# Kernel optimization log

Hardware: AMD Instinct MI355X
Metric: run time of the kernel (lower is better)

## Reference

```python
import jax, jax.numpy as jnp
import numpy as np

N, D, H, F = 50000, 128, 8, 512
HD = D // H
EPS_BN = 1e-5


def _batchnorm(x, gamma, beta):
    # BatchNorm1d in training mode: per-feature batch stats over node dim
    m = x.mean(axis=0)
    v = x.var(axis=0)
    return (x - m) * jax.lax.rsqrt(v + EPS_BN) * gamma + beta


def setup_inputs() -> dict:
    key = jax.random.key(0)
    ks = jax.random.split(key, 12)
    s = 0.05
    return {
        "src": jax.random.normal(ks[0], (N, D), jnp.float32),
        "edge_index": jax.random.randint(ks[1], (2, 800000), 0, N, jnp.int64),
        "q_w": jax.random.normal(ks[2], (D, D), jnp.float32) * s,
        "q_b": jnp.zeros((D,), jnp.float32),
        "k_w": jax.random.normal(ks[3], (D, D), jnp.float32) * s,
        "v_w": jax.random.normal(ks[4], (D, D), jnp.float32) * s,
        "out_w": jax.random.normal(ks[5], (D, D), jnp.float32) * s,
        "out_b": jnp.zeros((D,), jnp.float32),
        "g1": jnp.ones((D,), jnp.float32),
        "b1": jnp.zeros((D,), jnp.float32),
        "lin1_w": jax.random.normal(ks[6], (F, D), jnp.float32) * s,
        "lin1_b": jnp.zeros((F,), jnp.float32),
        "lin2_w": jax.random.normal(ks[7], (D, F), jnp.float32) * s,
        "lin2_b": jnp.zeros((D,), jnp.float32),
        "g2": jnp.ones((D,), jnp.float32),
        "b2": jnp.zeros((D,), jnp.float32),
    }


def reference(src, edge_index, q_w, q_b, k_w, v_w, out_w, out_b,
              g1, b1, lin1_w, lin1_b, lin2_w, lin2_b, g2, b2):
    n = src.shape[0]
    # add self loops, then attention edge index is (dst=edge[1], src=edge[0])
    loops = jnp.arange(n, dtype=edge_index.dtype)
    ei = jnp.concatenate([edge_index, jnp.stack([loops, loops])], axis=1)
    e_src, e_dst = ei[0], ei[1]  # message flows e_src -> e_dst; query index = e_dst

    scaling = float(HD) ** (-0.5)
    q = ((src @ q_w.T + q_b) * scaling).reshape(n, H, HD)
    k = (src @ k_w.T).reshape(n, H, HD)
    v = (src @ v_w.T).reshape(n, H, HD)

    # per-edge scores [E, H]
    w = jnp.einsum("ehd,ehd->eh", q[e_dst], k[e_src])
    # deterministic segment softmax over edges grouped by destination node
    mx = jax.ops.segment_max(w, e_dst, num_segments=n)
    ex = jnp.exp(w - mx[e_dst])
    den = jax.ops.segment_sum(ex, e_dst, num_segments=n)
    attn_w = ex / (den[e_dst] + 1e-16)  # [E, H]

    # weighted scatter-add aggregation -> [n, H, HD]
    msgs = attn_w[:, :, None] * v[e_src]
    agg = jax.ops.segment_sum(msgs, e_dst, num_segments=n)

    attn_out = agg.reshape(n, D) @ out_w.T + out_b
    x = _batchnorm(src + attn_out, g1, b1)

    ff = jax.nn.leaky_relu(x @ lin1_w.T + lin1_b, negative_slope=0.01)
    ff = ff @ lin2_w.T + lin2_b
    x = _batchnorm(x + ff, g2, b2)
    return x
```

## Files before the change

### kernel.cpp

```cpp
#include <hip/hip_runtime.h>
#include <math.h>

#define D 128
#define H 8
#define HD 16

typedef __attribute__((ext_vector_type(8))) short bf16x8;
typedef __attribute__((ext_vector_type(4))) float f32x4;

__device__ __forceinline__ ushort f2bf(float x) {
    union { float f; unsigned u; } v; v.f = x;
    unsigned r = v.u + 0x7fffu + ((v.u >> 16) & 1u);
    return (ushort)(r >> 16);
}
__device__ __forceinline__ float bflo(unsigned u) {
    union { unsigned u; float f; } x; x.u = u << 16; return x.f;
}
__device__ __forceinline__ float bfhi(unsigned u) {
    union { unsigned u; float f; } x; x.u = u & 0xffff0000u; return x.f;
}
__device__ __forceinline__ float bf2f(short s) {
    union { unsigned u; float f; } x; x.u = ((unsigned)(ushort)s) << 16; return x.f;
}

__device__ __forceinline__ float dot16(const float* qf, uint4 a, uint4 b) {
    float w;
    w  = qf[0]  * bflo(a.x) + qf[1]  * bfhi(a.x);
    w += qf[2]  * bflo(a.y) + qf[3]  * bfhi(a.y);
    w += qf[4]  * bflo(a.z) + qf[5]  * bfhi(a.z);
    w += qf[6]  * bflo(a.w) + qf[7]  * bfhi(a.w);
    w += qf[8]  * bflo(b.x) + qf[9]  * bfhi(b.x);
    w += qf[10] * bflo(b.y) + qf[11] * bfhi(b.y);
    w += qf[12] * bflo(b.z) + qf[13] * bfhi(b.z);
    w += qf[14] * bflo(b.w) + qf[15] * bfhi(b.w);
    return w;
}
__device__ __forceinline__ void acc16(float* num, float e, uint4 a, uint4 b) {
    num[0]  = fmaf(e, bflo(a.x), num[0]);  num[1]  = fmaf(e, bfhi(a.x), num[1]);
    num[2]  = fmaf(e, bflo(a.y), num[2]);  num[3]  = fmaf(e, bfhi(a.y), num[3]);
    num[4]  = fmaf(e, bflo(a.z), num[4]);  num[5]  = fmaf(e, bfhi(a.z), num[5]);
    num[6]  = fmaf(e, bflo(a.w), num[6]);  num[7]  = fmaf(e, bfhi(a.w), num[7]);
    num[8]  = fmaf(e, bflo(b.x), num[8]);  num[9]  = fmaf(e, bfhi(b.x), num[9]);
    num[10] = fmaf(e, bflo(b.y), num[10]); num[11] = fmaf(e, bfhi(b.y), num[11]);
    num[12] = fmaf(e, bflo(b.z), num[12]); num[13] = fmaf(e, bfhi(b.z), num[13]);
    num[14] = fmaf(e, bflo(b.w), num[14]); num[15] = fmaf(e, bfhi(b.w), num[15]);
}

template<int AMODE, int EPI, int K, int MW>
__global__ __launch_bounds__(256)
void gemm_v2_kernel(const void* __restrict__ Ap,
                    const ushort* __restrict__ W,
                    const float* __restrict__ bias,
                    const void* __restrict__ extra,
                    const float* __restrict__ stats,
                    ushort* __restrict__ outb,
                    int N)
{
    constexpr int M   = MW * 4;
    constexpr int KC  = (K < 128) ? K : 128;
    constexpr int KT  = KC / 32;
    constexpr int NKC = K / KC;

    const int lane = threadIdx.x & 63, wave = threadIdx.x >> 6;
    const int lr = lane & 15, lq = lane >> 4;
    const int row0 = blockIdx.x * 32;
    const int c0w  = wave * MW;

    int ar0 = row0 + lr;      if (ar0 > N - 1) ar0 = N - 1;
    int ar1 = row0 + 16 + lr; if (ar1 > N - 1) ar1 = N - 1;

    bf16x8 afr[2][KT];

    auto loadA = [&](int kc) {
        #pragma unroll
        for (int s = 0; s < 2; ++s) {
            int ar = s ? ar1 : ar0;
            if (AMODE == 0 || AMODE == 2) {
                const ushort* ap = (const ushort*)Ap + (size_t)ar * K + kc * KC + lq * 8;
                #pragma unroll
                for (int t = 0; t < KT; ++t) {
                    bf16x8 raw = *(const bf16x8*)(ap + t * 32);
                    if (AMODE == 0) {
                        afr[s][t] = raw;
                    } else {
                        int kb = kc * KC + t * 32 + lq * 8;
                        const float4* scp = (const float4*)(stats + 256 + kb);
                        const float4* shp = (const float4*)(stats + 384 + kb);
                        float4 sA = scp[0], sB = scp[1], hA = shp[0], hB = shp[1];
                        bf16x8 o;
                        o[0] = (short)f2bf(fmaf(bf2f(raw[0]), sA.x, hA.x));
                        o[1] = (short)f2bf(fmaf(bf2f(raw[1]), sA.y, hA.y));
                        o[2] = (short)f2bf(fmaf(bf2f(raw[2]), sA.z, hA.z));
                        o[3] = (short)f2bf(fmaf(bf2f(raw[3]), sA.w, hA.w));
                        o[4] = (short)f2bf(fmaf(bf2f(raw[4]), sB.x, hB.x));
                        o[5] = (short)f2bf(fmaf(bf2f(raw[5]), sB.y, hB.y));
                        o[6] = (short)f2bf(fmaf(bf2f(raw[6]), sB.z, hB.z));
                        o[7] = (short)f2bf(fmaf(bf2f(raw[7]), sB.w, hB.w));
                        afr[s][t] = o;
                    }
                }
            } else {
                const float* ap = (const float*)Ap + (size_t)ar * K + kc * KC + lq * 8;
                #pragma unroll
                for (int t = 0; t < KT; ++t) {
                    float4 f0 = *(const float4*)(ap + t * 32);
                    float4 f1 = *(const float4*)(ap + t * 32 + 4);
                    bf16x8 o;
                    o[0] = (short)f2bf(f0.x); o[1] = (short)f2bf(f0.y);
                    o[2] = (short)f2bf(f0.z); o[3] = (short)f2bf(f0.w);
                    o[4] = (short)f2bf(f1.x); o[5] = (short)f2bf(f1.y);
                    o[6] = (short)f2bf(f1.z); o[7] = (short)f2bf(f1.w);
                    afr[s][t] = o;
                }
            }
        }
    };

    if (NKC == 1) loadA(0);

    const float*  extf = (const float*)extra;
    const ushort* extb = (const ushort*)extra;

    #pragma unroll 1
    for (int cp = 0; cp < MW / 32; ++cp) {
        const int cbase = c0w + cp * 32;
        f32x4 acc[2][2] = {};

        #pragma unroll 1
        for (int kc = 0; kc < NKC; ++kc) {
            if (NKC > 1) loadA(kc);
            const ushort* wp0 = W + (size_t)(cbase + lr) * K + kc * KC + lq * 8;
            const ushort* wp1 = wp0 + (size_t)16 * K;
            #pragma unroll
            for (int t = 0; t < KT; ++t) {
                bf16x8 b0 = *(const bf16x8*)(wp0 + t * 32);
                bf16x8 b1 = *(const bf16x8*)(wp1 + t * 32);
                acc[0][0] = __builtin_amdgcn_mfma_f32_16x16x32_bf16(afr[0][t], b0, acc[0][0], 0, 0, 0);
                acc[1][0] = __builtin_amdgcn_mfma_f32_16x16x32_bf16(afr[1][t], b0, acc[1][0], 0, 0, 0);
                acc[0][1] = __builtin_amdgcn_mfma_f32_16x16x32_bf16(afr[0][t], b1, acc[0][1], 0, 0, 0);
                acc[1][1] = __builtin_amdgcn_mfma_f32_16x16x32_bf16(afr[1][t], b1, acc[1][1], 0, 0, 0);
            }
        }

        #pragma unroll
        for (int ct = 0; ct < 2; ++ct) {
            int col = cbase + ct * 16 + lr;
            float biasv = bias[col];
            float scv = 0.f, shv = 0.f;
            if (EPI == 4) { scv = stats[256 + col]; shv = stats[384 + col]; }
            #pragma unroll
            for (int s = 0; s < 2; ++s) {
                #pragma unroll
                for (int r = 0; r < 4; ++r) {
                    int grow = row0 + s * 16 + lq * 4 + r;
                    if (grow >= N) continue;
                    size_t o = (size_t)grow * M + col;
                    float v = acc[s][ct][r] + biasv;
                    if (EPI == 2) {
                        v = v > 0.f ? v : 0.01f * v;
                    } else if (EPI == 3) {
                        v += extf[o];
                    } else if (EPI == 4) {
                        v += fmaf(bf2f((short)extb[o]), scv, shv);
                    }
                    outb[o] = f2bf(v);
                }
            }
        }
    }
}

__global__ __launch_bounds__(256)
void convert_weights_kernel(const float* __restrict__ qw, const float* __restrict__ qb,
                            const float* __restrict__ kw, const float* __restrict__ vw,
                            const float* __restrict__ ow, const float* __restrict__ w1,
                            const float* __restrict__ w2,
                            ushort* __restrict__ wqkv, ushort* __restrict__ wout,
                            ushort* __restrict__ w1b, ushort* __restrict__ w2b,
                            float* __restrict__ bqkv)
{
    int i = blockIdx.x * 256 + threadIdx.x;
    if (i < 49152) {
        int row = i >> 7;
        float v;
        if (row < 128)      v = 0.25f * qw[i];
        else if (row < 256) v = kw[i - 16384];
        else                v = vw[i - 32768];
        wqkv[i] = f2bf(v);
        return;
    }
    int j = i - 49152;
    if (j < 16384) { wout[j] = f2bf(ow[j]); return; }
    j -= 16384;
    if (j < 65536) { w1b[j] = f2bf(w1[j]); return; }
    j -= 65536;
    if (j < 65536) { w2b[j] = f2bf(w2[j]); return; }
    j -= 65536;
    if (j < 384) bqkv[j] = (j < 128) ? 0.25f * qb[j] : 0.f;
}

__global__ __launch_bounds__(256)
void deg_count_kernel(const int* __restrict__ ei, long long E0, int* __restrict__ deg)
{
    long long e = (long long)blockIdx.x * 256 + threadIdx.x;
    if (e < E0) atomicAdd(&deg[ei[E0 + e]], 1);
}

__global__ __launch_bounds__(256)
void scan_block_sum(const int* __restrict__ deg, int n, int* __restrict__ bsum)
{
    __shared__ int sh[256];
    int i = blockIdx.x * 256 + threadIdx.x;
    sh[threadIdx.x] = (i < n) ? deg[i] : 0;
    __syncthreads();
    for (int ofs = 128; ofs > 0; ofs >>= 1) {
        if (threadIdx.x < ofs) sh[threadIdx.x] += sh[threadIdx.x + ofs];
        __syncthreads();
    }
    if (threadIdx.x == 0) bsum[blockIdx.x] = sh[0];
}

__global__ void scan_offsets(const int* __restrict__ bsum, int nb, int* __restrict__ boff)
{
    __shared__ int sh[256];
    int v = (threadIdx.x < nb) ? bsum[threadIdx.x] : 0;
    sh[threadIdx.x] = v;
    __syncthreads();
    for (int ofs = 1; ofs < 256; ofs <<= 1) {
        int t = (threadIdx.x >= ofs) ? sh[threadIdx.x - ofs] : 0;
        __syncthreads();
        sh[threadIdx.x] += t;
        __syncthreads();
    }
    if (threadIdx.x < nb) boff[threadIdx.x] = sh[threadIdx.x] - v;
}

__global__ __launch_bounds__(256)
void scan_final(const int* __restrict__ deg, int n, const int* __restrict__ boff,
                int* __restrict__ rowptr)
{
    __shared__ int sh[256];
    int i = blockIdx.x * 256 + threadIdx.x;
    int v = (i < n) ? deg[i] : 0;
    sh[threadIdx.x] = v;
    __syncthreads();
    for (int ofs = 1; ofs < 256; ofs <<= 1) {
        int t = (threadIdx.x >= ofs) ? sh[threadIdx.x - ofs] : 0;
        __syncthreads();
        sh[threadIdx.x] += t;
        __syncthreads();
    }
    if (i < n) rowptr[i] = boff[blockIdx.x] + sh[threadIdx.x] - v;
    if (i == n - 1) rowptr[n] = boff[blockIdx.x] + sh[threadIdx.x];
}

__global__ __launch_bounds__(256)
void scatter_kernel(const int* __restrict__ ei, long long E0,
                    const int* __restrict__ rowptr, int* __restrict__ cnt,
                    int* __restrict__ col)
{
    long long e = (long long)blockIdx.x * 256 + threadIdx.x;
    if (e >= E0) return;
    int s = ei[e], d = ei[E0 + e];
    int pos = rowptr[d] + atomicAdd(&cnt[d], 1);
    col[pos] = s;
}

__global__ __launch_bounds__(256)
void gat_agg_kernel(const int* __restrict__ rowptr, const int* __restrict__ col,
                    const ushort* __restrict__ qkv, ushort* __restrict__ agg, int NH)
{
    int t = blockIdx.x * 256 + threadIdx.x;
    if (t >= NH) return;
    int node = t >> 3, h = t & 7;
    const uint4* Q = (const uint4*)qkv;

    const uint4* qp = Q + (size_t)node * 48 + h * 2;
    uint4 qa = qp[0], qb = qp[1];
    float qf[16];
    qf[0]=bflo(qa.x); qf[1]=bfhi(qa.x); qf[2]=bflo(qa.y); qf[3]=bfhi(qa.y);
    qf[4]=bflo(qa.z); qf[5]=bfhi(qa.z); qf[6]=bflo(qa.w); qf[7]=bfhi(qa.w);
    qf[8]=bflo(qb.x); qf[9]=bfhi(qb.x); qf[10]=bflo(qb.y); qf[11]=bfhi(qb.y);
    qf[12]=bflo(qb.z); qf[13]=bfhi(qb.z); qf[14]=bflo(qb.w); qf[15]=bfhi(qb.w);

    float num[16];
    #pragma unroll
    for (int i = 0; i < 16; i++) num[i] = 0.f;
    float den = 0.f;

    {
        uint4 ka = qp[16], kb = qp[17], va = qp[32], vb = qp[33];
        float e = __expf(dot16(qf, ka, kb));
        den += e; acc16(num, e, va, vb);
    }

    int beg = rowptr[node], end = rowptr[node + 1];
    int j = beg;
    for (; j + 4 <= end; j += 4) {
        int s0 = col[j], s1 = col[j+1], s2 = col[j+2], s3 = col[j+3];
        const uint4* b0 = Q + (size_t)s0 * 48 + h * 2;
        const uint4* b1 = Q + (size_t)s1 * 48 + h * 2;
        const uint4* b2 = Q + (size_t)s2 * 48 + h * 2;
        const uint4* b3 = Q + (size_t)s3 * 48 + h * 2;
        uint4 ka0=b0[16], kb0=b0[17], va0=b0[32], vb0=b0[33];
        uint4 ka1=b1[16], kb1=b1[17], va1=b1[32], vb1=b1[33];
        uint4 ka2=b2[16], kb2=b2[17], va2=b2[32], vb2=b2[33];
        uint4 ka3=b3[16], kb3=b3[17], va3=b3[32], vb3=b3[33];
        float e0 = __expf(dot16(qf, ka0, kb0));
        float e1 = __expf(dot16(qf, ka1, kb1));
        float e2 = __expf(dot16(qf, ka2, kb2));
        float e3 = __expf(dot16(qf, ka3, kb3));
        den += e0 + e1 + e2 + e3;
        acc16(num, e0, va0, vb0); acc16(num, e1, va1, vb1);
        acc16(num, e2, va2, vb2); acc16(num, e3, va3, vb3);
    }
    for (; j < end; ++j) {
        int s = col[j];
        const uint4* bp = Q + (size_t)s * 48 + h * 2;
        uint4 ka = bp[16], kb = bp[17], va = bp[32], vb = bp[33];
        float e = __expf(dot16(qf, ka, kb));
        den += e; acc16(num, e, va, vb);
    }

    float inv = 1.f / (den + 1e-16f);
    uint4 o0, o1;
    o0.x = (uint)f2bf(num[0]*inv)  | ((uint)f2bf(num[1]*inv)  << 16);
    o0.y = (uint)f2bf(num[2]*inv)  | ((uint)f2bf(num[3]*inv)  << 16);
    o0.z = (uint)f2bf(num[4]*inv)  | ((uint)f2bf(num[5]*inv)  << 16);
    o0.w = (uint)f2bf(num[6]*inv)  | ((uint)f2bf(num[7]*inv)  << 16);
    o1.x = (uint)f2bf(num[8]*inv)  | ((uint)f2bf(num[9]*inv)  << 16);
    o1.y = (uint)f2bf(num[10]*inv) | ((uint)f2bf(num[11]*inv) << 16);
    o1.z = (uint)f2bf(num[12]*inv) | ((uint)f2bf(num[13]*inv) << 16);
    o1.w = (uint)f2bf(num[14]*inv) | ((uint)f2bf(num[15]*inv) << 16);
    uint4* op = reinterpret_cast<uint4*>(agg + (size_t)node * 128 + h * 16);
    op[0] = o0; op[1] = o1;
}

__global__ __launch_bounds__(256)
void bn_stats_bf16_kernel(const ushort* __restrict__ y, int N, float* __restrict__ stats)
{
    int jp = threadIdx.x & 63;
    int q4 = threadIdx.x >> 6;
    int r = blockIdx.x * 256 + q4;
    int rend = min(N, (int)(blockIdx.x + 1) * 256);
    float s0 = 0.f, qq0 = 0.f, s1 = 0.f, qq1 = 0.f;
    const uint* yp = (const uint*)y;
    for (; r < rend; r += 4) {
        uint u = yp[(size_t)r * 64 + jp];
        float a = bflo(u), b = bfhi(u);
        s0 += a; qq0 += a * a; s1 += b; qq1 += b * b;
    }
    __shared__ float sh[4][64][4];
    sh[q4][jp][0] = s0; sh[q4][jp][1] = qq0; sh[q4][jp][2] = s1; sh[q4][jp][3] = qq1;
    __syncthreads();
    if (threadIdx.x < 128) {
        int p = threadIdx.x >> 1;
        int w = threadIdx.x & 1;
        float ss = 0.f, sq = 0.f;
        #pragma unroll
        for (int i = 0; i < 4; i++) { ss += sh[i][p][w * 2]; sq += sh[i][p][w * 2 + 1]; }
        unsafeAtomicAdd(&stats[2 * p + w], ss);
        unsafeAtomicAdd(&stats[128 + 2 * p + w], sq);
    }
}

__global__ void bn_finalize_kernel(float* __restrict__ stats,
                                   const float* __restrict__ g,
                                   const float* __restrict__ b, int N)
{
    int j = threadIdx.x;
    float mean = stats[j] / (float)N;
    float var  = stats[128 + j] / (float)N - mean * mean;
    float sc = g[j] * rsqrtf(var + 1e-5f);
    stats[256 + j] = sc;
    stats[384 + j] = b[j] - mean * sc;
}

__global__ __launch_bounds__(256)
void bn_apply_out_kernel(const ushort* __restrict__ y, const float* __restrict__ stats,
                         float* __restrict__ out, int total4)
{
    int i = blockIdx.x * 256 + threadIdx.x;
    if (i >= total4) return;
    uint2 u = reinterpret_cast<const uint2*>(y)[i];
    int j = (i * 4) & (D - 1);
    float4 v;
    v.x = bflo(u.x) * stats[256 + j + 0] + stats[384 + j + 0];
    v.y = bfhi(u.x) * stats[256 + j + 1] + stats[384 + j + 1];
    v.z = bflo(u.y) * stats[256 + j + 2] + stats[384 + j + 2];
    v.w = bfhi(u.y) * stats[256 + j + 3] + stats[384 + j + 3];
    reinterpret_cast<float4*>(out)[i] = v;
}

extern "C" void kernel_launch(void* const* d_in, const int* in_sizes, int n_in,
                              void* d_out, int out_size, void* d_ws, size_t ws_size,
                              hipStream_t stream)
{
    const float* src    = (const float*)d_in[0];
    const int*   ei     = (const int*)  d_in[1];
    const float* q_w    = (const float*)d_in[2];
    const float* q_b    = (const float*)d_in[3];
    const float* k_w    = (const float*)d_in[4];
    const float* v_w    = (const float*)d_in[5];
    const float* out_w  = (const float*)d_in[6];
    const float* out_b  = (const float*)d_in[7];
    const float* g1     = (const float*)d_in[8];
    const float* b1     = (const float*)d_in[9];
    const float* lin1_w = (const float*)d_in[10];
    const float* lin1_b = (const float*)d_in[11];
    const float* lin2_w = (const float*)d_in[12];
    const float* lin2_b = (const float*)d_in[13];
    const float* g2     = (const float*)d_in[14];
    const float* b2     = (const float*)d_in[15];

    const int N        = in_sizes[0] / D;
    const long long E0 = in_sizes[1] / 2;

    float* ws = (float*)d_ws;
    size_t off = 0;
    ushort* qkv  = (ushort*)(ws + off); off += (size_t)N * 192;
    ushort* agg  = (ushort*)(ws + off); off += (size_t)N * 64;
    ushort* y1b  = (ushort*)(ws + off); off += (size_t)N * 64;
    ushort* hid  = (ushort*)(ws + off); off += (size_t)N * 256;
    ushort* y2b  = (ushort*)(ws + off); off += (size_t)N * 64;
    ushort* wqkv = (ushort*)(ws + off); off += 24576;
    ushort* woutb= (ushort*)(ws + off); off += 8192;
    ushort* w1b  = (ushort*)(ws + off); off += 32768;
    ushort* w2b  = (ushort*)(ws + off); off += 32768;
    float*  bqkv = ws + off;            off += 384;
    size_t zero_start = off;
    int* deg    = (int*)(ws + off); off += N;
    int* cnt    = (int*)(ws + off); off += N;
    float* stats1 = ws + off; off += 512;
    float* stats2 = ws + off; off += 512;
    size_t zero_cnt = off - zero_start;
    int* rowptr = (int*)(ws + off); off += N + 1;
    int* bsum   = (int*)(ws + off); off += 256;
    int* boff   = (int*)(ws + off); off += 256;
    int* col    = (int*)(ws + off); off += E0;

    hipMemsetAsync(ws + zero_start, 0, zero_cnt * sizeof(float), stream);

    dim3 blk(256);

    int cw_total = 49152 + 16384 + 65536 + 65536 + 384;
    hipLaunchKernelGGL(convert_weights_kernel, dim3((cw_total + 255) / 256), blk, 0, stream,
                       q_w, q_b, k_w, v_w, out_w, lin1_w, lin2_w,
                       wqkv, woutb, w1b, w2b, bqkv);

    dim3 gE0((unsigned)((E0 + 255) / 256));
    hipLaunchKernelGGL(deg_count_kernel, gE0, blk, 0, stream, ei, E0, deg);
    int nb = (N + 255) / 256;
    hipLaunchKernelGGL(scan_block_sum, dim3(nb), blk, 0, stream, deg, N, bsum);
    hipLaunchKernelGGL(scan_offsets, dim3(1), blk, 0, stream, bsum, nb, boff);
    hipLaunchKernelGGL(scan_final, dim3(nb), blk, 0, stream, deg, N, boff, rowptr);
    hipLaunchKernelGGL(scatter_kernel, gE0, blk, 0, stream, ei, E0, rowptr, cnt, col);

    dim3 gG((N + 31) / 32);

    hipLaunchKernelGGL((gemm_v2_kernel<1, 0, 128, 96>), gG, blk, 0, stream,
                       src, wqkv, bqkv, nullptr, nullptr, qkv, N);

    int NH = N * H;
    hipLaunchKernelGGL(gat_agg_kernel, dim3((NH + 255) / 256), blk, 0, stream,
                       rowptr, col, qkv, agg, NH);

    hipLaunchKernelGGL((gemm_v2_kernel<0, 3, 128, 32>), gG, blk, 0, stream,
                       agg, woutb, out_b, src, nullptr, y1b, N);

    dim3 gS((N + 255) / 256);
    hipLaunchKernelGGL(bn_stats_bf16_kernel, gS, blk, 0, stream, y1b, N, stats1);
    hipLaunchKernelGGL(bn_finalize_kernel, dim3(1), dim3(128), 0, stream, stats1, g1, b1, N);

    hipLaunchKernelGGL((gemm_v2_kernel<2, 2, 128, 128>), gG, blk, 0, stream,
                       y1b, w1b, lin1_b, nullptr, stats1, hid, N);
    hipLaunchKernelGGL((gemm_v2_kernel<0, 4, 512, 32>), gG, blk, 0, stream,
                       hid, w2b, lin2_b, y1b, stats1, y2b, N);

    hipLaunchKernelGGL(bn_stats_bf16_kernel, gS, blk, 0, stream, y2b, N, stats2);
    hipLaunchKernelGGL(bn_finalize_kernel, dim3(1), dim3(128), 0, stream, stats2, g2, b2, N);
    int total4 = N * D / 4;
    hipLaunchKernelGGL(bn_apply_out_kernel, dim3((total4 + 255) / 256), blk, 0, stream,
                       y2b, stats2, (float*)d_out, total4);
}
```

Baseline: 477.2 us.

## Split each node's edges across eight lane groups and fuse the scan kernels

```diff
diff --git a/kernel.cpp b/kernel.cpp
--- a/kernel.cpp
+++ b/kernel.cpp
@@ -66,8 +66,8 @@
     const int row0 = blockIdx.x * 32;
     const int c0w  = wave * MW;
 
-    int ar0 = row0 + lr;      if (ar0 > N - 1) ar0 = N - 1;
-    int ar1 = row0 + 16 + lr; if (ar1 > N - 1) ar1 = N - 1;
+    int ar0 = min(row0 + lr, N - 1);
+    int ar1 = min(row0 + 16 + lr, N - 1);
 
     bf16x8 afr[2][KT];
 
@@ -220,38 +220,35 @@
     if (threadIdx.x == 0) bsum[blockIdx.x] = sh[0];
 }
 
-__global__ void scan_offsets(const int* __restrict__ bsum, int nb, int* __restrict__ boff)
-{
+__global__ __launch_bounds__(256)
+void scan_final(const int* __restrict__ deg, int n, const int* __restrict__ bsum,
+                int nb, int* __restrict__ rowptr)
+{
+    __shared__ int sb[256];
     __shared__ int sh[256];
-    int v = (threadIdx.x < nb) ? bsum[threadIdx.x] : 0;
-    sh[threadIdx.x] = v;
+    int t = threadIdx.x;
+    sb[t] = (t < nb) ? bsum[t] : 0;
     __syncthreads();
     for (int ofs = 1; ofs < 256; ofs <<= 1) {
-        int t = (threadIdx.x >= ofs) ? sh[threadIdx.x - ofs] : 0;
+        int v = (t >= ofs) ? sb[t - ofs] : 0;
         __syncthreads();
-        sh[threadIdx.x] += t;
+        sb[t] += v;
         __syncthreads();
     }
-    if (threadIdx.x < nb) boff[threadIdx.x] = sh[threadIdx.x] - v;
-}
-
-__global__ __launch_bounds__(256)
-void scan_final(const int* __restrict__ deg, int n, const int* __restrict__ boff,
-                int* __restrict__ rowptr)
-{
-    __shared__ int sh[256];
-    int i = blockIdx.x * 256 + threadIdx.x;
+    int boff = (blockIdx.x == 0) ? 0 : sb[blockIdx.x - 1];
+
+    int i = blockIdx.x * 256 + t;
     int v = (i < n) ? deg[i] : 0;
-    sh[threadIdx.x] = v;
+    sh[t] = v;
     __syncthreads();
     for (int ofs = 1; ofs < 256; ofs <<= 1) {
-        int t = (threadIdx.x >= ofs) ? sh[threadIdx.x - ofs] : 0;
+        int u = (t >= ofs) ? sh[t - ofs] : 0;
         __syncthreads();
-        sh[threadIdx.x] += t;
+        sh[t] += u;
         __syncthreads();
     }
-    if (i < n) rowptr[i] = boff[blockIdx.x] + sh[threadIdx.x] - v;
-    if (i == n - 1) rowptr[n] = boff[blockIdx.x] + sh[threadIdx.x];
+    if (i < n) rowptr[i] = boff + sh[t] - v;
+    if (i == n - 1) rowptr[n] = boff + sh[t];
 }
 
 __global__ __launch_bounds__(256)
@@ -268,11 +265,12 @@
 
 __global__ __launch_bounds__(256)
 void gat_agg_kernel(const int* __restrict__ rowptr, const int* __restrict__ col,
-                    const ushort* __restrict__ qkv, ushort* __restrict__ agg, int NH)
-{
-    int t = blockIdx.x * 256 + threadIdx.x;
-    if (t >= NH) return;
-    int node = t >> 3, h = t & 7;
+                    const ushort* __restrict__ qkv, ushort* __restrict__ agg, int N)
+{
+    int node = blockIdx.x * 4 + (threadIdx.x >> 6);
+    if (node >= N) return;
+    int lane = threadIdx.x & 63;
+    int es = lane >> 3, h = lane & 7;
     const uint4* Q = (const uint4*)qkv;
 
     const uint4* qp = Q + (size_t)node * 48 + h * 2;
@@ -288,52 +286,38 @@
     for (int i = 0; i < 16; i++) num[i] = 0.f;
     float den = 0.f;
 
-    {
-        uint4 ka = qp[16], kb = qp[17], va = qp[32], vb = qp[33];
-        float e = __expf(dot16(qf, ka, kb));
-        den += e; acc16(num, e, va, vb);
-    }
-
-    int beg = rowptr[node], end = rowptr[node + 1];
-    int j = beg;
-    for (; j + 4 <= end; j += 4) {
-        int s0 = col[j], s1 = col[j+1], s2 = col[j+2], s3 = col[j+3];
-        const uint4* b0 = Q + (size_t)s0 * 48 + h * 2;
-        const uint4* b1 = Q + (size_t)s1 * 48 + h * 2;
-        const uint4* b2 = Q + (size_t)s2 * 48 + h * 2;
-        const uint4* b3 = Q + (size_t)s3 * 48 + h * 2;
-        uint4 ka0=b0[16], kb0=b0[17], va0=b0[32], vb0=b0[33];
-        uint4 ka1=b1[16], kb1=b1[17], va1=b1[32], vb1=b1[33];
-        uint4 ka2=b2[16], kb2=b2[17], va2=b2[32], vb2=b2[33];
-        uint4 ka3=b3[16], kb3=b3[17], va3=b3[32], vb3=b3[33];
-        float e0 = __expf(dot16(qf, ka0, kb0));
-        float e1 = __expf(dot16(qf, ka1, kb1));
-        float e2 = __expf(dot16(qf, ka2, kb2));
-        float e3 = __expf(dot16(qf, ka3, kb3));
-        den += e0 + e1 + e2 + e3;
-        acc16(num, e0, va0, vb0); acc16(num, e1, va1, vb1);
-        acc16(num, e2, va2, vb2); acc16(num, e3, va3, vb3);
-    }
-    for (; j < end; ++j) {
-        int s = col[j];
-        const uint4* bp = Q + (size_t)s * 48 + h * 2;
-        uint4 ka = bp[16], kb = bp[17], va = bp[32], vb = bp[33];
-        float e = __expf(dot16(qf, ka, kb));
-        den += e; acc16(num, e, va, vb);
-    }
-
-    float inv = 1.f / (den + 1e-16f);
-    uint4 o0, o1;
-    o0.x = (uint)f2bf(num[0]*inv)  | ((uint)f2bf(num[1]*inv)  << 16);
-    o0.y = (uint)f2bf(num[2]*inv)  | ((uint)f2bf(num[3]*inv)  << 16);
-    o0.z = (uint)f2bf(num[4]*inv)  | ((uint)f2bf(num[5]*inv)  << 16);
-    o0.w = (uint)f2bf(num[6]*inv)  | ((uint)f2bf(num[7]*inv)  << 16);
-    o1.x = (uint)f2bf(num[8]*inv)  | ((uint)f2bf(num[9]*inv)  << 16);
-    o1.y = (uint)f2bf(num[10]*inv) | ((uint)f2bf(num[11]*inv) << 16);
-    o1.z = (uint)f2bf(num[12]*inv) | ((uint)f2bf(num[13]*inv) << 16);
-    o1.w = (uint)f2bf(num[14]*inv) | ((uint)f2bf(num[15]*inv) << 16);
-    uint4* op = reinterpret_cast<uint4*>(agg + (size_t)node * 128 + h * 16);
-    op[0] = o0; op[1] = o1;
+    int beg = rowptr[node];
+    int total = rowptr[node + 1] - beg + 1;
+    for (int idx = es; idx < total; idx += 8) {
+        int s = (idx == 0) ? node : col[beg + idx - 1];
+        const uint4* rp = Q + (size_t)s * 48 + h * 2;
+        uint4 ka = rp[16], kb = rp[17], va = rp[32], vb = rp[33];
+        float ev = __expf(dot16(qf, ka, kb));
+        den += ev;
+        acc16(num, ev, va, vb);
+    }
+
+    #pragma unroll
+    for (int m = 8; m < 64; m <<= 1) {
+        den += __shfl_xor(den, m, 64);
+        #pragma unroll
+        for (int i = 0; i < 16; i++) num[i] += __shfl_xor(num[i], m, 64);
+    }
+
+    if (es == 0) {
+        float inv = 1.f / (den + 1e-16f);
+        uint4 o0, o1;
+        o0.x = (uint)f2bf(num[0]*inv)  | ((uint)f2bf(num[1]*inv)  << 16);
+        o0.y = (uint)f2bf(num[2]*inv)  | ((uint)f2bf(num[3]*inv)  << 16);
+        o0.z = (uint)f2bf(num[4]*inv)  | ((uint)f2bf(num[5]*inv)  << 16);
+        o0.w = (uint)f2bf(num[6]*inv)  | ((uint)f2bf(num[7]*inv)  << 16);
+        o1.x = (uint)f2bf(num[8]*inv)  | ((uint)f2bf(num[9]*inv)  << 16);
+        o1.y = (uint)f2bf(num[10]*inv) | ((uint)f2bf(num[11]*inv) << 16);
+        o1.z = (uint)f2bf(num[12]*inv) | ((uint)f2bf(num[13]*inv) << 16);
+        o1.w = (uint)f2bf(num[14]*inv) | ((uint)f2bf(num[15]*inv) << 16);
+        uint4* op = (uint4*)(agg + (size_t)node * 128 + h * 16);
+        op[0] = o0; op[1] = o1;
+    }
 }
 
 __global__ __launch_bounds__(256)
@@ -436,7 +420,6 @@
     size_t zero_cnt = off - zero_start;
     int* rowptr = (int*)(ws + off); off += N + 1;
     int* bsum   = (int*)(ws + off); off += 256;
-    int* boff   = (int*)(ws + off); off += 256;
     int* col    = (int*)(ws + off); off += E0;
 
     hipMemsetAsync(ws + zero_start, 0, zero_cnt * sizeof(float), stream);
@@ -452,8 +435,7 @@
     hipLaunchKernelGGL(deg_count_kernel, gE0, blk, 0, stream, ei, E0, deg);
     int nb = (N + 255) / 256;
     hipLaunchKernelGGL(scan_block_sum, dim3(nb), blk, 0, stream, deg, N, bsum);
-    hipLaunchKernelGGL(scan_offsets, dim3(1), blk, 0, stream, bsum, nb, boff);
-    hipLaunchKernelGGL(scan_final, dim3(nb), blk, 0, stream, deg, N, boff, rowptr);
+    hipLaunchKernelGGL(scan_final, dim3(nb), blk, 0, stream, deg, N, bsum, nb, rowptr);
     hipLaunchKernelGGL(scatter_kernel, gE0, blk, 0, stream, ei, E0, rowptr, cnt, col);
 
     dim3 gG((N + 31) / 32);
@@ -461,9 +443,8 @@
     hipLaunchKernelGGL((gemm_v2_kernel<1, 0, 128, 96>), gG, blk, 0, stream,
                        src, wqkv, bqkv, nullptr, nullptr, qkv, N);
 
-    int NH = N * H;
-    hipLaunchKernelGGL(gat_agg_kernel, dim3((NH + 255) / 256), blk, 0, stream,
-                       rowptr, col, qkv, agg, NH);
+    hipLaunchKernelGGL(gat_agg_kernel, dim3((N + 3) / 4), blk, 0, stream,
+                       rowptr, col, qkv, agg, N);
 
     hipLaunchKernelGGL((gemm_v2_kernel<0, 3, 128, 32>), gG, blk, 0, stream,
                        agg, woutb, out_b, src, nullptr, y1b, N);
```

New measurement: 470.0 us. About the same (-1.5%).
